# Performance work log

Measured on AMD Instinct MI355X. Metric: run time of the kernel, lower is better.

Reference implementation:

```python
import jax, jax.numpy as jnp
import numpy as np

B, T, H = 4, 4096, 2048
G_EPS = 0.5
LN_EPS = 1e-5
INIT_STD = 0.02


def setup_inputs() -> dict:
    key = jax.random.key(0)
    ks = jax.random.split(key, 4)
    return {
        "hidden_states": jax.random.normal(ks[0], (B, T, H), jnp.float32),
        "W_z": jax.random.normal(ks[1], (H, H), jnp.float32) * INIT_STD,
        "b_z": jnp.zeros((H,), jnp.float32),
        "W_h": jax.random.normal(ks[2], (H, H), jnp.float32) * INIT_STD,
        "b_h": jnp.zeros((H,), jnp.float32),
        "ln_w": jnp.ones((H,), jnp.float32),
        "ln_b": jnp.zeros((H,), jnp.float32),
        "h0": jax.random.normal(ks[3], (H,), jnp.float32) * INIT_STD,
    }


def _g_log(x):
    # torch.where(x >= 0, log(relu(x) + g_eps), -softplus(-x))
    return jnp.where(x >= 0, jnp.log(jax.nn.relu(x) + G_EPS), -jax.nn.softplus(-x))


def reference(hidden_states, W_z, b_z, W_h, b_h, ln_w, ln_b, h0):
    Bc, Tc, Hc = hidden_states.shape
    k = hidden_states @ W_z.T + b_z                      # [B,T,H]
    log_z = -jax.nn.softplus(-k)                         # log sigmoid(k)
    log_coeffs = -jax.nn.softplus(k)                     # log(1 - sigmoid(k))
    log_tilde_h = _g_log(hidden_states @ W_h.T + b_h)    # [B,T,H]
    log_h0 = jnp.broadcast_to(_g_log(h0), (Bc, 1, Hc))
    log_values = jnp.concatenate([log_h0, log_z + log_tilde_h], axis=1)  # [B,T+1,H]
    # NOTE: faithful to source: cumsum over the LAST (hidden) dim, then pad one
    # zero row at the front of the time dim (F.pad(..., (0,0,1,0))).
    a_star = jnp.pad(jnp.cumsum(log_coeffs, axis=-1), ((0, 0), (1, 0), (0, 0)))  # [B,T+1,H]
    log_h = a_star + jax.lax.cumlogsumexp(log_values - a_star, axis=1)
    # global mean / unbiased std normalization, as in source
    log_h = (log_h - log_h.mean()) / jnp.std(log_h, ddof=1)
    h = jnp.exp(log_h)[:, 1:, :]                         # drop the h0 step
    # residual + LayerNorm (dropout is identity in eval)
    x = h + hidden_states
    mu = x.mean(axis=-1, keepdims=True)
    var = x.var(axis=-1, keepdims=True)
    return (x - mu) * jax.lax.rsqrt(var + LN_EPS) * ln_w + ln_b
```

## Files before the change

kernel.cpp:

```cpp
#include <hip/hip_runtime.h>
#include <stdint.h>

constexpr int NB = 4;
constexpr int NT = 4096;
constexpr int NH = 2048;
constexpr int MROWS = NB * NT;
constexpr int TP1 = NT + 1;
constexpr int CH2 = 16;
constexpr int NCH2 = (TP1 + CH2 - 1) / CH2;

typedef unsigned short u16;
typedef __bf16 bf16x8 __attribute__((ext_vector_type(8)));
typedef float f32x4 __attribute__((ext_vector_type(4)));
typedef unsigned short u16x8 __attribute__((ext_vector_type(8)));
typedef u16x8 __attribute__((may_alias)) u16x8_a;
typedef float4 __attribute__((may_alias)) float4_a;

__device__ __forceinline__ u16 f2bf(float f) {
  unsigned int u = __float_as_uint(f);
  return (u16)((u + 0x7fffu + ((u >> 16) & 1u)) >> 16);
}
__device__ __forceinline__ float bf2f(u16 v) {
  return __uint_as_float(((unsigned int)v) << 16);
}
__device__ __forceinline__ float spf_(float x) {
  return fmaxf(x, 0.f) + __logf(1.f + __expf(-fabsf(x)));
}
__device__ __forceinline__ float glogf_(float x) {
  return (x >= 0.f) ? __logf(x + 0.5f) : -spf_(-x);
}
__device__ __forceinline__ void gld16(const void* g, void* l) {
  __builtin_amdgcn_global_load_lds((const __attribute__((address_space(1))) void*)g,
                                   (__attribute__((address_space(3))) void*)l, 16, 0, 0);
}
__device__ __forceinline__ void ld8(const float* p, float* r) {
  float4 a = *(const float4_a*)p, b = *(const float4_a*)(p + 4);
  r[0] = a.x; r[1] = a.y; r[2] = a.z; r[3] = a.w;
  r[4] = b.x; r[5] = b.y; r[6] = b.z; r[7] = b.w;
}
__device__ __forceinline__ void st8(float* p, const float* r) {
  *(float4_a*)p       = make_float4(r[0], r[1], r[2], r[3]);
  *(float4_a*)(p + 4) = make_float4(r[4], r[5], r[6], r[7]);
}

__global__ __launch_bounds__(256) void cvt_all(
    const float* __restrict__ hs, const float* __restrict__ Wz,
    const float* __restrict__ Wh, u16* __restrict__ hsb,
    u16* __restrict__ wzb, u16* __restrict__ whb) {
  const int s0 = MROWS * NH / 8;
  const int s1 = s0 + NH * NH / 8;
  const int s2 = s1 + NH * NH / 8;
  int i = blockIdx.x * 256 + threadIdx.x;
  if (i >= s2) return;
  const float* in; u16* out; int j;
  if (i < s0)      { in = hs; out = hsb; j = i; }
  else if (i < s1) { in = Wz; out = wzb; j = i - s0; }
  else             { in = Wh; out = whb; j = i - s1; }
  const float4* p = (const float4*)in;
  float4 a = p[2 * (size_t)j], b = p[2 * (size_t)j + 1];
  u16x8 o;
  o[0] = f2bf(a.x); o[1] = f2bf(a.y); o[2] = f2bf(a.z); o[3] = f2bf(a.w);
  o[4] = f2bf(b.x); o[5] = f2bf(b.y); o[6] = f2bf(b.z); o[7] = f2bf(b.w);
  *(u16x8*)(out + (size_t)j * 8) = o;
}

__global__ __launch_bounds__(256, 3) void gemm_bt(
    const u16* __restrict__ A,
    const u16* __restrict__ Bz, const u16* __restrict__ Bh,
    const float* __restrict__ bz, const float* __restrict__ bh,
    u16* __restrict__ KU) {
  const u16* Bm  = blockIdx.y ? Bh : Bz;
  const float* bias = blockIdx.y ? bh : bz;
  u16* Cw = KU + (blockIdx.y ? 2048 : 0);

  const int bid = blockIdx.x;
  const int wg = (bid & 7) * 256 + (bid >> 3);
  const int bx = wg & 15;
  const int by = wg >> 4;
  const int row0 = by << 7, col0 = bx << 7;

  __shared__ u16 ldsA[128 * 64];
  __shared__ u16 ldsB[128 * 64];

  const int tid = threadIdx.x;
  const int lane = tid & 63;
  const int wv = tid >> 6;
  const int wr = (wv >> 1) << 6;
  const int wc = (wv & 1) << 6;

  const int srow = lane >> 3;
  const int sslot = ((lane & 7) ^ srow) << 3;
  const int xsw = (lane & 7) << 3;
  const int q8 = (lane >> 4) << 3;
  const int f15 = lane & 15;

  f32x4 acc[4][4] = {};

  for (int k0 = 0; k0 < NH; k0 += 64) {
    if (k0) __syncthreads();
#pragma unroll
    for (int i = 0; i < 4; ++i) {
      const int r = i * 32 + wv * 8 + srow;
      const size_t gcol = (size_t)(k0 + sslot);
      gld16(A  + (size_t)(row0 + r) * NH + gcol, &ldsA[(size_t)(i * 256 + wv * 64) * 8]);
      gld16(Bm + (size_t)(col0 + r) * NH + gcol, &ldsB[(size_t)(i * 256 + wv * 64) * 8]);
    }
    __syncthreads();
#pragma unroll
    for (int ks = 0; ks < 2; ++ks) {
      const int cphys = ((ks << 5) | q8) ^ xsw;
      bf16x8 af[4], bfr[4];
#pragma unroll
      for (int m = 0; m < 4; ++m)
        af[m] = *(const bf16x8*)&ldsA[(wr + m * 16 + f15) * 64 + cphys];
#pragma unroll
      for (int n = 0; n < 4; ++n)
        bfr[n] = *(const bf16x8*)&ldsB[(wc + n * 16 + f15) * 64 + cphys];
#pragma unroll
      for (int m = 0; m < 4; ++m)
#pragma unroll
        for (int n = 0; n < 4; ++n)
          acc[m][n] = __builtin_amdgcn_mfma_f32_16x16x32_bf16(af[m], bfr[n], acc[m][n], 0, 0, 0);
    }
  }

  const int fr = lane & 15, fq = lane >> 4;
#pragma unroll
  for (int n = 0; n < 4; ++n) {
    const int col = col0 + wc + n * 16 + fr;
    const float bv = bias[col];
#pragma unroll
    for (int m = 0; m < 4; ++m) {
#pragma unroll
      for (int v = 0; v < 4; ++v) {
        const int row = row0 + wr + m * 16 + fq * 4 + v;
        Cw[(size_t)row * 4096 + col] = f2bf(acc[m][n][v] + bv);
      }
    }
  }
}

__device__ __forceinline__ void row_pointwise(const char* KU, size_t row,
                                              int tid, float* lc, float* lv) {
  const size_t rb = row * 8192;
  u16x8 kv = *(const u16x8_a*)(KU + rb + tid * 16);
  u16x8 uv = *(const u16x8_a*)(KU + rb + 4096 + tid * 16);
#pragma unroll
  for (int e = 0; e < 8; ++e) {
    const float k = bf2f(kv[e]);
    const float L = __logf(1.f + __expf(-fabsf(k)));
    lc[e] = -fmaxf(k, 0.f) - L;
    lv[e] = fminf(k, 0.f) - L + glogf_(bf2f(uv[e]));
  }
}

__global__ __launch_bounds__(256) void carry_pass(
    const char* __restrict__ KU, float* __restrict__ cm, float* __restrict__ cs,
    const float* __restrict__ h0) {
  const int ch = blockIdx.x;
  const int b = blockIdx.y;
  const int tid = threadIdx.x;
  const int lane = tid & 63, wvx = tid >> 6;
  const int t0 = ch * CH2;
  const int t1 = (t0 + CH2 < TP1) ? (t0 + CH2) : TP1;

  float m8[8], s8[8];
#pragma unroll
  for (int e = 0; e < 8; ++e) { m8[e] = -INFINITY; s8[e] = 0.f; }

  __shared__ float wsum[2][4];

  float lc[8], lv[8];
  {
    const int tf = (t0 < 1) ? 1 : t0;
    if (tf < t1) row_pointwise(KU, (size_t)b * NT + (tf - 1), tid, lc, lv);
  }

  for (int tt = t0; tt < t1; ++tt) {
    if (tt == 0) {
#pragma unroll
      for (int e = 0; e < 8; ++e) {
        const float x = glogf_(h0[tid * 8 + e]);
        m8[e] = x; s8[e] = 1.f;
      }
      continue;
    }
    float nlc[8], nlv[8];
    const bool pf = (tt + 1 < t1);
    if (pf) row_pointwise(KU, (size_t)b * NT + tt, tid, nlc, nlv);

    float cum[8], run = 0.f;
#pragma unroll
    for (int e = 0; e < 8; ++e) { run += lc[e]; cum[e] = run; }
    float v = run;
#pragma unroll
    for (int d = 1; d < 64; d <<= 1) {
      float o = __shfl_up(v, d, 64);
      if (lane >= d) v += o;
    }
    const int par = tt & 1;
    if (lane == 63) wsum[par][wvx] = v;
    __syncthreads();
    float base = v - run;
#pragma unroll
    for (int w = 0; w < 4; ++w)
      if (w < wvx) base += wsum[par][w];

#pragma unroll
    for (int e = 0; e < 8; ++e) {
      const float x = lv[e] - (base + cum[e]);
      const float nm = fmaxf(m8[e], x);
      s8[e] = s8[e] * __expf(m8[e] - nm) + __expf(x - nm);
      m8[e] = nm;
    }
    if (pf) {
#pragma unroll
      for (int e = 0; e < 8; ++e) { lc[e] = nlc[e]; lv[e] = nlv[e]; }
    }
  }
  const size_t co = ((size_t)ch * NB + b) * NH + tid * 8;
  st8(cm + co, m8);
  st8(cs + co, s8);
}

__global__ __launch_bounds__(256) void carryscan(float* __restrict__ cm,
                                                 float* __restrict__ cs) {
  const int c = blockIdx.x * 256 + threadIdx.x;
  const int b = c >> 11;
  const int hh = c & (NH - 1);
  float Cm = -INFINITY, Cs = 0.f;
  size_t o = ((size_t)0 * NB + b) * NH + hh;
  float m2 = cm[o], s2 = cs[o];
  for (int ch = 0; ch < NCH2; ++ch) {
    float nm2, ns2;
    if (ch + 1 < NCH2) {
      const size_t on = ((size_t)(ch + 1) * NB + b) * NH + hh;
      nm2 = cm[on]; ns2 = cs[on];
    }
    cm[o] = Cm; cs[o] = Cs;
    const float M = fmaxf(Cm, m2);
    Cs = Cs * __expf(Cm - M) + s2 * __expf(m2 - M);
    Cm = M;
    o = ((size_t)(ch + 1) * NB + b) * NH + hh;
    m2 = nm2; s2 = ns2;
  }
}

__global__ __launch_bounds__(256) void scan_final(
    const char* __restrict__ KU, float* __restrict__ LH,
    const float* __restrict__ cm, const float* __restrict__ cs,
    const float* __restrict__ h0, double* __restrict__ sums) {
  const int ch = blockIdx.x;
  const int b = blockIdx.y;
  const int tid = threadIdx.x;
  const int lane = tid & 63, wvx = tid >> 6;
  const int t0 = ch * CH2;
  const int t1 = (t0 + CH2 < TP1) ? (t0 + CH2) : TP1;

  float m8[8], s8[8];
  {
    const size_t co = ((size_t)ch * NB + b) * NH + tid * 8;
    ld8(cm + co, m8);
    ld8(cs + co, s8);
  }

  __shared__ float wsum[2][4];
  double s1 = 0.0, s2 = 0.0;

  float lc[8], lv[8];
  {
    const int tf = (t0 < 1) ? 1 : t0;
    if (tf < t1) row_pointwise(KU, (size_t)b * NT + (tf - 1), tid, lc, lv);
  }

  for (int tt = t0; tt < t1; ++tt) {
    if (tt == 0) {
#pragma unroll
      for (int e = 0; e < 8; ++e) {
        const float x = glogf_(h0[tid * 8 + e]);
        m8[e] = x; s8[e] = 1.f;
        s1 += (double)x;
        s2 += (double)x * (double)x;
      }
      continue;
    }
    float nlc[8], nlv[8];
    const bool pf = (tt + 1 < t1);
    if (pf) row_pointwise(KU, (size_t)b * NT + tt, tid, nlc, nlv);

    float cum[8], run = 0.f;
#pragma unroll
    for (int e = 0; e < 8; ++e) { run += lc[e]; cum[e] = run; }
    float v = run;
#pragma unroll
    for (int d = 1; d < 64; d <<= 1) {
      float o = __shfl_up(v, d, 64);
      if (lane >= d) v += o;
    }
    const int par = tt & 1;
    if (lane == 63) wsum[par][wvx] = v;
    __syncthreads();
    float base = v - run;
#pragma unroll
    for (int w = 0; w < 4; ++w)
      if (w < wvx) base += wsum[par][w];

    float lh8[8];
#pragma unroll
    for (int e = 0; e < 8; ++e) {
      const float as = base + cum[e];
      const float x = lv[e] - as;
      const float nm = fmaxf(m8[e], x);
      s8[e] = s8[e] * __expf(m8[e] - nm) + __expf(x - nm);
      m8[e] = nm;
      const float lh = as + nm + __logf(s8[e]);
      lh8[e] = lh;
      s1 += (double)lh;
      s2 += (double)lh * (double)lh;
    }
    st8(LH + ((size_t)b * NT + (tt - 1)) * NH + tid * 8, lh8);
    if (pf) {
#pragma unroll
      for (int e = 0; e < 8; ++e) { lc[e] = nlc[e]; lv[e] = nlv[e]; }
    }
  }
  double v1 = s1, v2 = s2;
#pragma unroll
  for (int d = 32; d; d >>= 1) {
    v1 += __shfl_down(v1, d, 64);
    v2 += __shfl_down(v2, d, 64);
  }
  __shared__ double dr1[4], dr2[4];
  if (lane == 0) { dr1[wvx] = v1; dr2[wvx] = v2; }
  __syncthreads();
  if (tid == 0) {
    atomicAdd(&sums[0], dr1[0] + dr1[1] + dr1[2] + dr1[3]);
    atomicAdd(&sums[1], dr2[0] + dr2[1] + dr2[2] + dr2[3]);
  }
}

__global__ void finalize_stats(const double* __restrict__ sums,
                               float* __restrict__ stats) {
  const double S = sums[0], S2 = sums[1];
  const double N = (double)NB * (double)TP1 * (double)NH;
  const double mu = S / N;
  const double var = (S2 - S * S / N) / (N - 1.0);
  stats[0] = (float)mu;
  stats[1] = (float)(1.0 / sqrt(var));
}

__global__ __launch_bounds__(256) void final_ln(float* __restrict__ LL,
                                                const float* __restrict__ hs,
                                                const float* __restrict__ lnw,
                                                const float* __restrict__ lnb,
                                                const float* __restrict__ stats) {
  const int tid = threadIdx.x;
  const size_t off = (size_t)blockIdx.x * NH + tid * 8;
  const float mu_g = stats[0], isd = stats[1];

  float lh[8], av[8];
  ld8(LL + off, lh);
  ld8(hs + off, av);
  float x[8];
  float s = 0.f, q = 0.f;
#pragma unroll
  for (int e = 0; e < 8; ++e) {
    x[e] = __expf((lh[e] - mu_g) * isd) + av[e];
    s += x[e];
    q += x[e] * x[e];
  }
#pragma unroll
  for (int d = 32; d; d >>= 1) {
    s += __shfl_down(s, d, 64);
    q += __shfl_down(q, d, 64);
  }
  __shared__ float r1[4], r2[4];
  const int lane = tid & 63, wvx = tid >> 6;
  if (lane == 0) { r1[wvx] = s; r2[wvx] = q; }
  __syncthreads();
  const float st = r1[0] + r1[1] + r1[2] + r1[3];
  const float qt = r2[0] + r2[1] + r2[2] + r2[3];
  const float mean = st * (1.0f / NH);
  const float var = qt * (1.0f / NH) - mean * mean;
  const float rstd = rsqrtf(var + 1e-5f);

  float wv8[8], bv8[8];
  ld8(lnw + tid * 8, wv8);
  ld8(lnb + tid * 8, bv8);
  float o[8];
#pragma unroll
  for (int e = 0; e < 8; ++e)
    o[e] = (x[e] - mean) * rstd * wv8[e] + bv8[e];
  st8(LL + off, o);
}

extern "C" void kernel_launch(void* const* d_in, const int* in_sizes, int n_in,
                              void* d_out, int out_size, void* d_ws, size_t ws_size,
                              hipStream_t stream) {
  (void)in_sizes; (void)n_in; (void)out_size; (void)ws_size;
  const float* hs  = (const float*)d_in[0];
  const float* Wz  = (const float*)d_in[1];
  const float* bz  = (const float*)d_in[2];
  const float* Wh  = (const float*)d_in[3];
  const float* bh  = (const float*)d_in[4];
  const float* lnw = (const float*)d_in[5];
  const float* lnb = (const float*)d_in[6];
  const float* h0  = (const float*)d_in[7];
  float* out = (float*)d_out;

  char* w = (char*)d_ws;
  u16* hsb   = (u16*)w;  w += (size_t)MROWS * NH * 2;
  u16* wzb   = (u16*)w;  w += (size_t)NH * NH * 2;
  u16* whb   = (u16*)w;  w += (size_t)NH * NH * 2;
  char* KU   = w;        w += (size_t)MROWS * 8192;
  double* sums = (double*)w; w += 16;
  float* stats = (float*)w;  w += 16;
  float* cm_ = (float*)hsb;
  float* cs_ = cm_ + (size_t)NCH2 * NB * NH;

  hipMemsetAsync(sums, 0, 16, stream);

  {
    const int tot8 = MROWS * NH / 8 + 2 * (NH * NH / 8);
    cvt_all<<<dim3((tot8 + 255) / 256), 256, 0, stream>>>(hs, Wz, Wh, hsb, wzb, whb);
  }

  gemm_bt<<<dim3((MROWS / 128) * (NH / 128), 2), 256, 0, stream>>>(
      hsb, wzb, whb, bz, bh, (u16*)KU);

  carry_pass<<<dim3(NCH2, NB), 256, 0, stream>>>(KU, cm_, cs_, h0);

  carryscan<<<dim3(NB * NH / 256), 256, 0, stream>>>(cm_, cs_);

  scan_final<<<dim3(NCH2, NB), 256, 0, stream>>>(KU, out, cm_, cs_, h0, sums);
  finalize_stats<<<1, 1, 0, stream>>>(sums, stats);

  final_ln<<<dim3(MROWS), 256, 0, stream>>>(out, hs, lnw, lnb, stats);
}
```

Baseline: 618.3 us.

## Double-buffer GEMM LDS, store log_h in fp16, read bf16 residual, retune scan chunks

The GEMM now uses two LDS buffers so the next K-tile's global-to-LDS load overlaps MFMA work on the current tile, with occupancy hint lowered to 2. When the workspace is large enough, the scan writes log_h as fp16 into a separate buffer and the LayerNorm reads it back, halving that intermediate traffic. The LayerNorm residual now comes from the bf16 copy of the hidden states instead of the fp32 input. The scan chunk length changes from 16 to 17 and the carry buffers move into the weight workspace. These cut memory traffic at the cost of lower precision in log_h and in the residual.

```diff
diff --git a/kernel.cpp b/kernel.cpp
--- a/kernel.cpp
+++ b/kernel.cpp
@@ -6,14 +6,17 @@
 constexpr int NH = 2048;
 constexpr int MROWS = NB * NT;
 constexpr int TP1 = NT + 1;
-constexpr int CH2 = 16;
-constexpr int NCH2 = (TP1 + CH2 - 1) / CH2;
+constexpr int CH2 = 17;
+constexpr int NCH2 = 241;
+constexpr int NKT = NH / 64;
 
 typedef unsigned short u16;
 typedef __bf16 bf16x8 __attribute__((ext_vector_type(8)));
 typedef float f32x4 __attribute__((ext_vector_type(4)));
 typedef unsigned short u16x8 __attribute__((ext_vector_type(8)));
+typedef _Float16 h16x8 __attribute__((ext_vector_type(8)));
 typedef u16x8 __attribute__((may_alias)) u16x8_a;
+typedef h16x8 __attribute__((may_alias)) h16x8_a;
 typedef float4 __attribute__((may_alias)) float4_a;
 
 __device__ __forceinline__ u16 f2bf(float f) {
@@ -64,7 +67,7 @@
   *(u16x8*)(out + (size_t)j * 8) = o;
 }
 
-__global__ __launch_bounds__(256, 3) void gemm_bt(
+__global__ __launch_bounds__(256, 2) void gemm_db(
     const u16* __restrict__ A,
     const u16* __restrict__ Bz, const u16* __restrict__ Bh,
     const float* __restrict__ bz, const float* __restrict__ bh,
@@ -79,8 +82,8 @@
   const int by = wg >> 4;
   const int row0 = by << 7, col0 = bx << 7;
 
-  __shared__ u16 ldsA[128 * 64];
-  __shared__ u16 ldsB[128 * 64];
+  __shared__ u16 ldsA[2][128 * 64];
+  __shared__ u16 ldsB[2][128 * 64];
 
   const int tid = threadIdx.x;
   const int lane = tid & 63;
@@ -94,35 +97,48 @@
   const int q8 = (lane >> 4) << 3;
   const int f15 = lane & 15;
 
+#define STAGE(sb, k0)                                                          \
+  _Pragma("unroll")                                                            \
+  for (int i_ = 0; i_ < 4; ++i_) {                                             \
+    const int r_ = i_ * 32 + wv * 8 + srow;                                    \
+    const size_t gc_ = (size_t)((k0) + sslot);                                 \
+    gld16(A  + (size_t)(row0 + r_) * NH + gc_,                                 \
+          &ldsA[sb][(size_t)(i_ * 256 + wv * 64) * 8]);                        \
+    gld16(Bm + (size_t)(col0 + r_) * NH + gc_,                                 \
+          &ldsB[sb][(size_t)(i_ * 256 + wv * 64) * 8]);                        \
+  }
+
   f32x4 acc[4][4] = {};
 
-  for (int k0 = 0; k0 < NH; k0 += 64) {
-    if (k0) __syncthreads();
-#pragma unroll
-    for (int i = 0; i < 4; ++i) {
-      const int r = i * 32 + wv * 8 + srow;
-      const size_t gcol = (size_t)(k0 + sslot);
-      gld16(A  + (size_t)(row0 + r) * NH + gcol, &ldsA[(size_t)(i * 256 + wv * 64) * 8]);
-      gld16(Bm + (size_t)(col0 + r) * NH + gcol, &ldsB[(size_t)(i * 256 + wv * 64) * 8]);
-    }
-    __syncthreads();
+  STAGE(0, 0);
+  __syncthreads();
+
+  int cur = 0;
+  for (int t = 0; t < NKT; ++t) {
+    if (t + 1 < NKT) { STAGE(cur ^ 1, (t + 1) << 6); }
+    __builtin_amdgcn_sched_barrier(0);
+    const u16* la = ldsA[cur];
+    const u16* lb = ldsB[cur];
 #pragma unroll
     for (int ks = 0; ks < 2; ++ks) {
       const int cphys = ((ks << 5) | q8) ^ xsw;
       bf16x8 af[4], bfr[4];
 #pragma unroll
       for (int m = 0; m < 4; ++m)
-        af[m] = *(const bf16x8*)&ldsA[(wr + m * 16 + f15) * 64 + cphys];
+        af[m] = *(const bf16x8*)&la[(wr + m * 16 + f15) * 64 + cphys];
 #pragma unroll
       for (int n = 0; n < 4; ++n)
-        bfr[n] = *(const bf16x8*)&ldsB[(wc + n * 16 + f15) * 64 + cphys];
+        bfr[n] = *(const bf16x8*)&lb[(wc + n * 16 + f15) * 64 + cphys];
 #pragma unroll
       for (int m = 0; m < 4; ++m)
 #pragma unroll
         for (int n = 0; n < 4; ++n)
           acc[m][n] = __builtin_amdgcn_mfma_f32_16x16x32_bf16(af[m], bfr[n], acc[m][n], 0, 0, 0);
     }
-  }
+    __syncthreads();
+    cur ^= 1;
+  }
+#undef STAGE
 
   const int fr = lane & 15, fq = lane >> 4;
 #pragma unroll
@@ -246,8 +262,10 @@
   }
 }
 
+template <int HLH>
 __global__ __launch_bounds__(256) void scan_final(
-    const char* __restrict__ KU, float* __restrict__ LH,
+    const char* __restrict__ KU, float* __restrict__ LH32,
+    _Float16* __restrict__ LH16,
     const float* __restrict__ cm, const float* __restrict__ cs,
     const float* __restrict__ h0, double* __restrict__ sums) {
   const int ch = blockIdx.x;
@@ -318,7 +336,15 @@
       s1 += (double)lh;
       s2 += (double)lh * (double)lh;
     }
-    st8(LH + ((size_t)b * NT + (tt - 1)) * NH + tid * 8, lh8);
+    const size_t row = (size_t)b * NT + (tt - 1);
+    if (HLH) {
+      h16x8 hv;
+#pragma unroll
+      for (int e = 0; e < 8; ++e) hv[e] = (_Float16)lh8[e];
+      *(h16x8_a*)(LH16 + row * NH + tid * 8) = hv;
+    } else {
+      st8(LH32 + row * NH + tid * 8, lh8);
+    }
     if (pf) {
 #pragma unroll
       for (int e = 0; e < 8; ++e) { lc[e] = nlc[e]; lv[e] = nlv[e]; }
@@ -349,18 +375,29 @@
   stats[1] = (float)(1.0 / sqrt(var));
 }
 
-__global__ __launch_bounds__(256) void final_ln(float* __restrict__ LL,
-                                                const float* __restrict__ hs,
-                                                const float* __restrict__ lnw,
-                                                const float* __restrict__ lnb,
-                                                const float* __restrict__ stats) {
+template <int HLH>
+__global__ __launch_bounds__(256) void final_ln(
+    float* __restrict__ OUT, const float* __restrict__ LH32,
+    const _Float16* __restrict__ LH16, const u16* __restrict__ hsb,
+    const float* __restrict__ lnw, const float* __restrict__ lnb,
+    const float* __restrict__ stats) {
   const int tid = threadIdx.x;
   const size_t off = (size_t)blockIdx.x * NH + tid * 8;
   const float mu_g = stats[0], isd = stats[1];
 
   float lh[8], av[8];
-  ld8(LL + off, lh);
-  ld8(hs + off, av);
+  if (HLH) {
+    h16x8 hv = *(const h16x8_a*)(LH16 + off);
+#pragma unroll
+    for (int e = 0; e < 8; ++e) lh[e] = (float)hv[e];
+  } else {
+    ld8(LH32 + off, lh);
+  }
+  {
+    u16x8 hv = *(const u16x8_a*)(hsb + off);
+#pragma unroll
+    for (int e = 0; e < 8; ++e) av[e] = bf2f(hv[e]);
+  }
   float x[8];
   float s = 0.f, q = 0.f;
 #pragma unroll
@@ -391,13 +428,13 @@
 #pragma unroll
   for (int e = 0; e < 8; ++e)
     o[e] = (x[e] - mean) * rstd * wv8[e] + bv8[e];
-  st8(LL + off, o);
+  st8(OUT + off, o);
 }
 
 extern "C" void kernel_launch(void* const* d_in, const int* in_sizes, int n_in,
                               void* d_out, int out_size, void* d_ws, size_t ws_size,
                               hipStream_t stream) {
-  (void)in_sizes; (void)n_in; (void)out_size; (void)ws_size;
+  (void)in_sizes; (void)n_in; (void)out_size;
   const float* hs  = (const float*)d_in[0];
   const float* Wz  = (const float*)d_in[1];
   const float* bz  = (const float*)d_in[2];
@@ -408,14 +445,18 @@
   const float* h0  = (const float*)d_in[7];
   float* out = (float*)d_out;
 
-  char* w = (char*)d_ws;
+  char* w0 = (char*)d_ws;
+  char* w = w0;
   u16* hsb   = (u16*)w;  w += (size_t)MROWS * NH * 2;
   u16* wzb   = (u16*)w;  w += (size_t)NH * NH * 2;
   u16* whb   = (u16*)w;  w += (size_t)NH * NH * 2;
   char* KU   = w;        w += (size_t)MROWS * 8192;
   double* sums = (double*)w; w += 16;
-  float* stats = (float*)w;  w += 16;
-  float* cm_ = (float*)hsb;
+  float* stats = (float*)w;  w += 64;
+  _Float16* LH16 = (_Float16*)w;
+  const size_t need_half = (size_t)(w - w0) + (size_t)MROWS * NH * 2;
+  const bool use_half = (ws_size >= need_half);
+  float* cm_ = (float*)wzb;
   float* cs_ = cm_ + (size_t)NCH2 * NB * NH;
 
   hipMemsetAsync(sums, 0, 16, stream);
@@ -425,15 +466,21 @@
     cvt_all<<<dim3((tot8 + 255) / 256), 256, 0, stream>>>(hs, Wz, Wh, hsb, wzb, whb);
   }
 
-  gemm_bt<<<dim3((MROWS / 128) * (NH / 128), 2), 256, 0, stream>>>(
+  gemm_db<<<dim3((MROWS / 128) * (NH / 128), 2), 256, 0, stream>>>(
       hsb, wzb, whb, bz, bh, (u16*)KU);
 
   carry_pass<<<dim3(NCH2, NB), 256, 0, stream>>>(KU, cm_, cs_, h0);
 
   carryscan<<<dim3(NB * NH / 256), 256, 0, stream>>>(cm_, cs_);
 
-  scan_final<<<dim3(NCH2, NB), 256, 0, stream>>>(KU, out, cm_, cs_, h0, sums);
+  if (use_half)
+    scan_final<1><<<dim3(NCH2, NB), 256, 0, stream>>>(KU, out, LH16, cm_, cs_, h0, sums);
+  else
+    scan_final<0><<<dim3(NCH2, NB), 256, 0, stream>>>(KU, out, LH16, cm_, cs_, h0, sums);
   finalize_stats<<<1, 1, 0, stream>>>(sums, stats);
 
-  final_ln<<<dim3(MROWS), 256, 0, stream>>>(out, hs, lnw, lnb, stats);
-}
+  if (use_half)
+    final_ln<1><<<dim3(MROWS), 256, 0, stream>>>(out, out, LH16, hsb, lnw, lnb, stats);
+  else
+    final_ln<0><<<dim3(MROWS), 256, 0, stream>>>(out, out, LH16, hsb, lnw, lnb, stats);
+}
```

Result: faster. 580.9 us (-6.0%).
